# Kernel tuning notes

Hardware: AMD Instinct MI355X
Metric: run time of the kernel (lower is better)

Reference implementation:

```python
import jax, jax.numpy as jnp
import numpy as np

K_NEIGHBORS = 5
WEIGHT = 0.5
EPS = 1e-12


def _l2_normalize(x):
    return x / jnp.maximum(jnp.linalg.norm(x, axis=1, keepdims=True), EPS)


def setup_inputs() -> dict:
    key = jax.random.key(0)
    k1, k2, k3, k4 = jax.random.split(key, 4)
    return {
        "hidden_current": jax.random.normal(k1, (4096, 768), dtype=jnp.float32),
        "hidden_previous": jax.random.normal(k2, (8192, 768), dtype=jnp.float32),
        "labels_current": jax.random.randint(k3, (4096,), 0, 100, dtype=jnp.int64),
        "labels_previous": jax.random.randint(k4, (8192,), 0, 100, dtype=jnp.int64),
    }


def reference(hidden_current, hidden_previous, labels_current, labels_previous):
    B_curr = hidden_current.shape[0]
    B_prev = hidden_previous.shape[0]

    # --- affinity from previous representations (no_grad in original) ---
    hp = _l2_normalize(jax.lax.stop_gradient(hidden_previous))
    dist_prev = 1.0 - hp @ hp.T                      # [B_prev, B_prev] cosine distance
    # smallest k+1 distances == largest k+1 of negated distances
    _, nbr = jax.lax.top_k(-dist_prev, K_NEIGHBORS + 1)
    nbr = nbr[:, 1:]                                 # drop self, [B_prev, K]
    same = labels_previous[:, None] == labels_previous[nbr]   # [B_prev, K]
    e = jnp.where(same, 1.0, -1.0).astype(jnp.float32)        # w - b
    rows = jnp.arange(B_prev)[:, None]
    affinity = jnp.zeros((B_prev, B_prev), dtype=jnp.float32).at[rows, nbr].set(e)

    # --- squared pairwise distances of normalized current representations ---
    hc = _l2_normalize(hidden_current)
    sq = jnp.sum(hc * hc, axis=1)
    d2 = jnp.maximum(sq[:, None] + sq[None, :] - 2.0 * (hc @ hc.T), 0.0)  # [B_curr, B_curr]

    loss = jnp.sum(affinity[:B_curr, :B_curr] * d2) / (B_curr * B_curr)
    return WEIGHT * loss
```

## Files before the change

### kernel.cpp

```cpp
#include <hip/hip_runtime.h>

#define BC 4096
#define BP 8192
#define D  768
#define KNB 5
#define TOPK 6
#define NT (BP / 128)

typedef __bf16 bf16x8 __attribute__((ext_vector_type(8)));
typedef float  f32x4  __attribute__((ext_vector_type(4)));

__device__ __forceinline__ unsigned short f2bf(float f) {
    unsigned int u = __float_as_uint(f);
    u += 0x7fffu + ((u >> 16) & 1u);
    return (unsigned short)(u >> 16);
}

__device__ __forceinline__ void gload16(const void* g, void* l) {
    __builtin_amdgcn_global_load_lds(
        (const __attribute__((address_space(1))) unsigned int*)g,
        (__attribute__((address_space(3))) unsigned int*)l, 16, 0, 0);
}

__device__ __forceinline__ void topk_insert(float v, int j, float* bv, int* bj) {
    #pragma unroll
    for (int q = TOPK - 1; q >= 1; q--) {
        bool up   = v > bv[q - 1];
        bool here = (v > bv[q]) && !up;
        bv[q] = up ? bv[q - 1] : (here ? v : bv[q]);
        bj[q] = up ? bj[q - 1] : (here ? j : bj[q]);
    }
    if (v > bv[0]) { bv[0] = v; bj[0] = j; }
}

__global__ __launch_bounds__(256) void k_norm(const float* __restrict__ hp,
                                              const float* __restrict__ hc,
                                              unsigned short* __restrict__ hpnb,
                                              float* __restrict__ hcn,
                                              float* __restrict__ sqout,
                                              float* __restrict__ out) {
    int b = blockIdx.x;
    int t = threadIdx.x;
    if (b == 0 && t == 0) out[0] = 0.0f;
    bool isP = (b < BP);
    int row = isP ? b : (b - BP);
    const float* xr = (isP ? hp : hc) + (size_t)row * D;
    float v0 = xr[t], v1 = xr[t + 256], v2 = xr[t + 512];
    float s = v0 * v0 + v1 * v1 + v2 * v2;
    #pragma unroll
    for (int off = 32; off; off >>= 1) s += __shfl_xor(s, off, 64);
    __shared__ float wsum[4];
    if ((t & 63) == 0) wsum[t >> 6] = s;
    __syncthreads();
    float tot = wsum[0] + wsum[1] + wsum[2] + wsum[3];
    float rinv = 1.0f / fmaxf(sqrtf(tot), 1e-12f);
    if (isP) {
        unsigned short* yr = hpnb + (size_t)row * D;
        int rx = (row & 7) << 3;
        yr[t ^ rx]         = f2bf(v0 * rinv);
        yr[(t + 256) ^ rx] = f2bf(v1 * rinv);
        yr[(t + 512) ^ rx] = f2bf(v2 * rinv);
    } else {
        float* yr = hcn + (size_t)row * D;
        yr[t] = v0 * rinv; yr[t + 256] = v1 * rinv; yr[t + 512] = v2 * rinv;
        if (t == 0) sqout[row] = tot * rinv * rinv;
    }
}

__global__ __launch_bounds__(256, 4) void k_simtop(const unsigned short* __restrict__ hp,
                                                   float* __restrict__ candv,
                                                   int* __restrict__ candi) {
    __shared__ char smem[32768];
    unsigned short* sA = (unsigned short*)smem;
    unsigned short* sB = sA + 128 * 64;
    float* sS = (float*)smem;
    float* mv = (float*)(smem + 17408);
    int*   mj = (int*)(smem + 17408 + 3072);

    const int t = threadIdx.x;
    const int l = t & 63;
    const int w = t >> 6;
    const int l15 = l & 15, quad = l >> 4;
    const int wr = w >> 1, wc = w & 1;
    const int ri = blockIdx.x, ci = blockIdx.y;

    const int srow = l >> 3, sch = l & 7;
    const unsigned short* Ag = hp + (size_t)(ri * 128 + w * 32 + srow) * D + sch * 8;
    const unsigned short* Bg = hp + (size_t)(ci * 128 + w * 32 + srow) * D + sch * 8;
    unsigned short* la = sA + (w * 32) * 64;
    unsigned short* lb = sB + (w * 32) * 64;

    f32x4 acc[4][4];
    #pragma unroll
    for (int i = 0; i < 4; i++)
        #pragma unroll
        for (int j = 0; j < 4; j++) acc[i][j] = (f32x4){0.f, 0.f, 0.f, 0.f};

    const int x7  = l15 & 7;
    const int ch0 = (quad ^ x7) * 16;
    const int ch1 = ((quad + 4) ^ x7) * 16;

    for (int kk = 0; kk < D; kk += 64) {
        __syncthreads();
        #pragma unroll
        for (int p = 0; p < 4; p++) {
            gload16(Ag + (size_t)(p * 8) * D + kk, la + (p * 8) * 64);
            gload16(Bg + (size_t)(p * 8) * D + kk, lb + (p * 8) * 64);
        }
        __syncthreads();
        #pragma unroll
        for (int ks = 0; ks < 2; ks++) {
            const int ch = ks ? ch1 : ch0;
            bf16x8 af[4], bfr[4];
            #pragma unroll
            for (int mi = 0; mi < 4; mi++)
                af[mi] = *(const bf16x8*)((const char*)sA + (wr * 64 + mi * 16 + l15) * 128 + ch);
            #pragma unroll
            for (int ni = 0; ni < 4; ni++)
                bfr[ni] = *(const bf16x8*)((const char*)sB + (wc * 64 + ni * 16 + l15) * 128 + ch);
            #pragma unroll
            for (int mi = 0; mi < 4; mi++)
                #pragma unroll
                for (int ni = 0; ni < 4; ni++)
                    acc[mi][ni] = __builtin_amdgcn_mfma_f32_16x16x32_bf16(af[mi], bfr[ni], acc[mi][ni], 0, 0, 0);
        }
    }

    float bv[TOPK]; int bj[TOPK];
    #pragma unroll
    for (int s = 0; s < TOPK; s++) { bv[s] = -1e30f; bj[s] = 0x7fffffff; }

    const int erow = t & 127, scb = (t >> 7) * 16;
    #pragma unroll
    for (int p = 0; p < 4; p++) {
        __syncthreads();
        if (wc == (p >> 1)) {
            const int ni0 = (p & 1) * 2;
            #pragma unroll
            for (int mi = 0; mi < 4; mi++)
                #pragma unroll
                for (int n2 = 0; n2 < 2; n2++) {
                    int colb = n2 * 16 + l15;
                    int rowb = wr * 64 + mi * 16 + quad * 4;
                    f32x4 v = acc[mi][ni0 + n2];
                    #pragma unroll
                    for (int r = 0; r < 4; r++) sS[(rowb + r) * 33 + colb] = v[r];
                }
        }
        __syncthreads();
        int jbase = ci * 128 + p * 32 + scb;
        for (int c = 0; c < 16; c++) {
            float v = sS[erow * 33 + scb + c];
            if (v > bv[TOPK - 1]) topk_insert(v, jbase + c, bv, bj);
        }
    }

    __syncthreads();
    if (t >= 128) {
        #pragma unroll
        for (int s = 0; s < TOPK; s++) { mv[(t - 128) * TOPK + s] = bv[s]; mj[(t - 128) * TOPK + s] = bj[s]; }
    }
    __syncthreads();
    if (t < 128) {
        #pragma unroll
        for (int s0 = 0; s0 < TOPK; s0++) {
            float v = mv[t * TOPK + s0];
            if (v > bv[TOPK - 1]) topk_insert(v, mj[t * TOPK + s0], bv, bj);
        }
        size_t o = ((size_t)(ri * 128 + t) * NT + ci) * TOPK;
        #pragma unroll
        for (int s = 0; s < TOPK; s++) { candv[o + s] = bv[s]; candi[o + s] = bj[s]; }
    }
}

__global__ __launch_bounds__(256) void k_mergeloss(const float* __restrict__ candv,
                                                   const int* __restrict__ candi,
                                                   const float* __restrict__ hcn,
                                                   const float* __restrict__ sq,
                                                   const int* __restrict__ labp,
                                                   float* __restrict__ out) {
    __shared__ float bsum[4];
    const int w = threadIdx.x >> 6, lane = threadIdx.x & 63;
    const int i = blockIdx.x * 4 + w;

    const float* cv = candv + ((size_t)i * NT + lane) * TOPK;
    const int*   cj = candi + ((size_t)i * NT + lane) * TOPK;
    float bv[TOPK]; int bj[TOPK];
    #pragma unroll
    for (int s = 0; s < TOPK; s++) { bv[s] = cv[s]; bj[s] = cj[s]; }

    #pragma unroll
    for (int off = 1; off < 64; off <<= 1) {
        float pv[TOPK]; int pj[TOPK];
        #pragma unroll
        for (int s = 0; s < TOPK; s++) {
            pv[s] = __shfl_xor(bv[s], off, 64);
            pj[s] = __shfl_xor(bj[s], off, 64);
        }
        bool ilow = (lane & off) == 0;
        float av[TOPK], iv[TOPK]; int aj[TOPK], ij[TOPK];
        #pragma unroll
        for (int s = 0; s < TOPK; s++) {
            av[s] = ilow ? bv[s] : pv[s];  aj[s] = ilow ? bj[s] : pj[s];
            iv[s] = ilow ? pv[s] : bv[s];  ij[s] = ilow ? pj[s] : bj[s];
        }
        #pragma unroll
        for (int s = 0; s < TOPK; s++)
            if (iv[s] > av[TOPK - 1]) topk_insert(iv[s], ij[s], av, aj);
        #pragma unroll
        for (int s = 0; s < TOPK; s++) { bv[s] = av[s]; bj[s] = aj[s]; }
    }

    const float* hi = hcn + (size_t)i * D;
    float4 h0 = *(const float4*)(hi + lane * 4);
    float4 h1 = *(const float4*)(hi + lane * 4 + 256);
    float4 h2 = *(const float4*)(hi + lane * 4 + 512);
    float sqi = sq[i];
    int li = labp[i];
    float part = 0.f;
    float base = 0.f;
    #pragma unroll
    for (int s = 1; s <= KNB; s++) {
        int j = bj[s];
        if (j >= BC) continue;
        const float* hj = hcn + (size_t)j * D;
        float4 g0 = *(const float4*)(hj + lane * 4);
        float4 g1 = *(const float4*)(hj + lane * 4 + 256);
        float4 g2 = *(const float4*)(hj + lane * 4 + 512);
        float d = h0.x * g0.x + h0.y * g0.y + h0.z * g0.z + h0.w * g0.w
                + h1.x * g1.x + h1.y * g1.y + h1.z * g1.z + h1.w * g1.w
                + h2.x * g2.x + h2.y * g2.y + h2.z * g2.z + h2.w * g2.w;
        float e = (li == labp[j]) ? 1.0f : -1.0f;
        part += e * (-2.0f) * d;
        if (lane == 0) base += e * (sqi + sq[j]);
    }
    part += base;
    #pragma unroll
    for (int off = 32; off; off >>= 1) part += __shfl_xor(part, off, 64);
    if (lane == 0) bsum[w] = part;
    __syncthreads();
    if (threadIdx.x == 0) {
        float s = bsum[0] + bsum[1] + bsum[2] + bsum[3];
        unsafeAtomicAdd(out, 0.5f * s / ((float)BC * (float)BC));
    }
}

extern "C" void kernel_launch(void* const* d_in, const int* in_sizes, int n_in,
                              void* d_out, int out_size, void* d_ws, size_t ws_size,
                              hipStream_t stream) {
    const float* hc   = (const float*)d_in[0];
    const float* hp   = (const float*)d_in[1];
    const int*   labp = (const int*)d_in[3];
    float* out = (float*)d_out;

    unsigned short* hpnb = (unsigned short*)d_ws;
    float* hcn  = (float*)(hpnb + (size_t)BP * D);
    float* sq   = hcn + (size_t)BC * D;
    float* candv = sq + BC;
    int*   candi = (int*)(candv + (size_t)BC * NT * TOPK);

    k_norm<<<dim3(BP + BC), dim3(256), 0, stream>>>(hp, hc, hpnb, hcn, sq, out);
    k_simtop<<<dim3(BC / 128, NT), dim3(256), 0, stream>>>(hpnb, candv, candi);
    k_mergeloss<<<dim3(BC / 4), dim3(256), 0, stream>>>(candv, candi, hcn, sq, labp, out);
}
```

Before: 185.9 us.

## Exploit Gram matrix symmetry to compute only upper-triangle tiles in top-k search

The similarity kernel previously computed all 32x64 tiles of the 4096x8192 Gram slice. Tiles with both row and column blocks inside the first 4096 rows are now computed once as an upper triangle. Each off-diagonal tile also does a second, transposed top-k pass to produce candidates for the mirrored tile, while tiles against columns 4096..8191 are still computed in full. This cuts the matmul work by about a quarter, at the cost of extra epilogue work on triangle blocks, uneven per-block load, and lowering launch bounds occupancy from 4 to 3.

```diff
diff --git a/kernel.cpp b/kernel.cpp
--- a/kernel.cpp
+++ b/kernel.cpp
@@ -6,6 +6,7 @@
 #define KNB 5
 #define TOPK 6
 #define NT (BP / 128)
+#define NBLK 1552
 
 typedef __bf16 bf16x8 __attribute__((ext_vector_type(8)));
 typedef float  f32x4  __attribute__((ext_vector_type(4)));
@@ -67,7 +68,7 @@
     }
 }
 
-__global__ __launch_bounds__(256, 4) void k_simtop(const unsigned short* __restrict__ hp,
+__global__ __launch_bounds__(256, 3) void k_simtop(const unsigned short* __restrict__ hp,
                                                    float* __restrict__ candv,
                                                    int* __restrict__ candi) {
     __shared__ char smem[32768];
@@ -82,7 +83,17 @@
     const int w = t >> 6;
     const int l15 = l & 15, quad = l >> 4;
     const int wr = w >> 1, wc = w & 1;
-    const int ri = blockIdx.x, ci = blockIdx.y;
+
+    int ri, ci; bool tri;
+    {
+        int idx = blockIdx.x;
+        if (idx < 1024) { ri = idx >> 5; ci = 32 + (idx & 31); tri = false; }
+        else {
+            int r = idx - 1024, a = 0;
+            while (r >= 32 - a) { r -= 32 - a; a++; }
+            ri = a; ci = a + r; tri = (ri != ci);
+        }
+    }
 
     const int srow = l >> 3, sch = l & 7;
     const unsigned short* Ag = hp + (size_t)(ri * 128 + w * 32 + srow) * D + sch * 8;
@@ -154,7 +165,6 @@
             if (v > bv[TOPK - 1]) topk_insert(v, jbase + c, bv, bj);
         }
     }
-
     __syncthreads();
     if (t >= 128) {
         #pragma unroll
@@ -170,6 +180,50 @@
         size_t o = ((size_t)(ri * 128 + t) * NT + ci) * TOPK;
         #pragma unroll
         for (int s = 0; s < TOPK; s++) { candv[o + s] = bv[s]; candi[o + s] = bj[s]; }
+    }
+
+    if (tri) {
+        #pragma unroll
+        for (int s = 0; s < TOPK; s++) { bv[s] = -1e30f; bj[s] = 0x7fffffff; }
+        #pragma unroll
+        for (int p = 0; p < 4; p++) {
+            __syncthreads();
+            if (wr == (p >> 1)) {
+                const int mi0 = (p & 1) * 2;
+                #pragma unroll
+                for (int m2 = 0; m2 < 2; m2++)
+                    #pragma unroll
+                    for (int ni = 0; ni < 4; ni++) {
+                        int co = wc * 64 + ni * 16 + l15;
+                        int lr = m2 * 16 + quad * 4;
+                        f32x4 v = acc[mi0 + m2][ni];
+                        #pragma unroll
+                        for (int r = 0; r < 4; r++) sS[co * 33 + lr + r] = v[r];
+                    }
+            }
+            __syncthreads();
+            int jbase = ri * 128 + p * 32 + scb;
+            for (int c = 0; c < 16; c++) {
+                float v = sS[erow * 33 + scb + c];
+                if (v > bv[TOPK - 1]) topk_insert(v, jbase + c, bv, bj);
+            }
+        }
+        __syncthreads();
+        if (t >= 128) {
+            #pragma unroll
+            for (int s = 0; s < TOPK; s++) { mv[(t - 128) * TOPK + s] = bv[s]; mj[(t - 128) * TOPK + s] = bj[s]; }
+        }
+        __syncthreads();
+        if (t < 128) {
+            #pragma unroll
+            for (int s0 = 0; s0 < TOPK; s0++) {
+                float v = mv[t * TOPK + s0];
+                if (v > bv[TOPK - 1]) topk_insert(v, mj[t * TOPK + s0], bv, bj);
+            }
+            size_t o = ((size_t)(ci * 128 + t) * NT + ri) * TOPK;
+            #pragma unroll
+            for (int s = 0; s < TOPK; s++) { candv[o + s] = bv[s]; candi[o + s] = bj[s]; }
+        }
     }
 }
 
@@ -260,6 +314,6 @@
     int*   candi = (int*)(candv + (size_t)BC * NT * TOPK);
 
     k_norm<<<dim3(BP + BC), dim3(256), 0, stream>>>(hp, hc, hpnb, hcn, sq, out);
-    k_simtop<<<dim3(BC / 128, NT), dim3(256), 0, stream>>>(hpnb, candv, candi);
+    k_simtop<<<dim3(NBLK), dim3(256), 0, stream>>>(hpnb, candv, candi);
     k_mergeloss<<<dim3(BC / 4), dim3(256), 0, stream>>>(candv, candi, hcn, sq, labp, out);
 }
```

Measured after the change: 202.7 us. 1.09x slower.
